# Kernel optimization log

Measured on AMD Instinct MI355X. Metric: run time of the kernel, lower is better.

Reference implementation:

```python
import jax, jax.numpy as jnp
import numpy as np
from jax import lax

KH, KW = 3, 3  # hardcoded in the original extract_patches sizes=(1,3,3,1)


def setup_inputs() -> dict:
    key = jax.random.key(0)
    k1, k2, k3 = jax.random.split(key, 3)
    B, H, W, C = 32, 56, 56, 128
    num_och = 256
    x = jax.random.normal(k1, (B, H, W, C), dtype=jnp.float32)
    w = jax.random.normal(k2, (num_och, KH * KW * C), dtype=jnp.float32) * 0.05
    b = jax.random.normal(k3, (num_och,), dtype=jnp.float32) * 0.05
    return {"x": x, "w": w, "b": b}


def reference(x, w, b):
    # Original: extract_patches (SAME, stride 1, 3x3) -> tile num_och times ->
    # elementwise multiply with w -> reduce_sum over patch axis -> + bias.
    # This is exactly a 3x3 SAME conv: patch layout is (ky, kx, cin) row-major,
    # matching tf.image.extract_patches depth ordering.
    num_och = w.shape[0]
    cin = x.shape[-1]
    # (num_och, KH*KW*C) -> (KH, KW, C, num_och) for HWIO kernel layout
    kernel = w.reshape(num_och, KH, KW, cin).transpose(1, 2, 3, 0)
    out = lax.conv_general_dilated(
        x, kernel,
        window_strides=(1, 1),
        padding="SAME",
        dimension_numbers=("NHWC", "HWIO", "NHWC"),
    )
    return out + b
```

## Files before the change

kernel.cpp:

```cpp
#include <hip/hip_runtime.h>
#include <hip/hip_bf16.h>

#define HH   56
#define WW_  56
#define CIN  128
#define OCH  256
#define NPIX (32*56*56)
#define NX   (NPIX*CIN)
#define NW   (OCH*9*CIN)
#define XB_BYTES ((size_t)NX*2)
#define WB_BYTES ((size_t)NW*2)
#define ZP_OFF   (XB_BYTES + WB_BYTES)
#define WS_NEEDED (ZP_OFF + 256)

#define NT   18
#define SLOT 32768
#define THREADS 512

typedef __attribute__((ext_vector_type(8))) short bf16x8;
typedef __attribute__((ext_vector_type(4))) float f32x4;
typedef __attribute__((address_space(1))) void v_g;
typedef __attribute__((address_space(3))) void v_l;

__device__ __forceinline__ unsigned short f2bf(float f) {
  union { float f; unsigned u; } v; v.f = f;
  unsigned r = v.u + 0x7FFF + ((v.u >> 16) & 1);
  return (unsigned short)(r >> 16);
}

__global__ __launch_bounds__(256) void convert_kern(
    const float* __restrict__ x, const float* __restrict__ w,
    char* __restrict__ ws)
{
  if (blockIdx.x == 0 && threadIdx.x < 64)
    ((float*)(ws + ZP_OFF))[threadIdx.x] = 0.f;

  unsigned short* out = (unsigned short*)ws;
  const int NT8 = (NX + NW) / 8;
  for (int i = blockIdx.x * blockDim.x + threadIdx.x; i < NT8;
       i += gridDim.x * blockDim.x) {
    const int e = i * 8;
    const float* src = (e < NX) ? (x + e) : (w + (e - NX));
    const float4 a = ((const float4*)src)[0];
    const float4 b = ((const float4*)src)[1];
    union { bf16x8 v; unsigned short u[8]; } p;
    p.u[0] = f2bf(a.x); p.u[1] = f2bf(a.y); p.u[2] = f2bf(a.z); p.u[3] = f2bf(a.w);
    p.u[4] = f2bf(b.x); p.u[5] = f2bf(b.y); p.u[6] = f2bf(b.z); p.u[7] = f2bf(b.w);
    *(bf16x8*)(out + e) = p.v;
  }
}

__global__ __launch_bounds__(THREADS, 2) void conv_gemm3(
    const char* __restrict__ ws, const float* __restrict__ bias,
    float* __restrict__ out)
{
  __shared__ char lds[3 * SLOT];

  const char* xb = ws;
  const char* wb = ws + XB_BYTES;
  const char* zp = ws + ZP_OFF;

  const int tid  = threadIdx.x;
  const int lane = tid & 63;
  const int m0   = (blockIdx.x >> 1) * 128;
  const int n0   = (blockIdx.x & 1) * 128;

  const int r0  = tid >> 3;
  const int chk = ((tid & 7) ^ (r0 & 7)) * 16;
  const char* zpc = zp + chk;

  int pixA[2], phA[2], pwA[2];
  const char* bsrc[2];
#pragma unroll
  for (int l = 0; l < 2; ++l) {
    const int r  = r0 + l * 64;
    const int p  = m0 + r;
    const int pb = p / 3136;
    const int phw = p - pb * 3136;
    phA[l] = phw / 56;
    pwA[l] = phw - phA[l] * 56;
    pixA[l] = p;
    bsrc[l] = wb + (size_t)(n0 + r) * 2304 + chk;
  }

  const int fr = lane & 15;
  const int fq = lane >> 4;
  const int wv = tid >> 6;
  const int wr = wv >> 2;
  const int wc = wv & 3;

  int aoff[2][4], boff[2][2];
#pragma unroll
  for (int ks = 0; ks < 2; ++ks) {
#pragma unroll
    for (int mi = 0; mi < 4; ++mi) {
      const int r = wr * 64 + mi * 16 + fr;
      aoff[ks][mi] = r * 128 + ((ks * 64 + fq * 16) ^ ((r & 7) << 4));
    }
#pragma unroll
    for (int nj = 0; nj < 2; ++nj) {
      const int c = wc * 32 + nj * 16 + fr;
      boff[ks][nj] = 16384 + c * 128 + ((ks * 64 + fq * 16) ^ ((c & 7) << 4));
    }
  }

  f32x4 acc[4][2];
  const f32x4 zero4 = {0.f, 0.f, 0.f, 0.f};
#pragma unroll
  for (int mi = 0; mi < 4; ++mi)
#pragma unroll
    for (int nj = 0; nj < 2; ++nj) acc[mi][nj] = zero4;

#define STAGE(tt, dst) do {                                                   \
    const int kpos_ = (tt) >> 1, kh_ = (tt) & 1;                              \
    const int ky_ = kpos_ / 3;                                                \
    const int dy_ = ky_ - 1, dx_ = kpos_ - ky_ * 3 - 1;                       \
    _Pragma("unroll")                                                         \
    for (int l = 0; l < 2; ++l) {                                             \
      const int ih_ = phA[l] + dy_, iw_ = pwA[l] + dx_;                       \
      const bool v_ = ((unsigned)ih_ < 56u) & ((unsigned)iw_ < 56u);          \
      const char* ga_ = v_ ? (xb + (size_t)(pixA[l] + dy_ * 56 + dx_) * 256   \
                                 + kh_ * 128 + chk)                           \
                           : zpc;                                             \
      __builtin_amdgcn_global_load_lds((const v_g*)ga_,                       \
          (v_l*)((dst) + l * 8192 + tid * 16), 16, 0, 0);                     \
    }                                                                         \
    _Pragma("unroll")                                                         \
    for (int l = 0; l < 2; ++l)                                               \
      __builtin_amdgcn_global_load_lds((const v_g*)(bsrc[l] + (tt) * 128),    \
          (v_l*)((dst) + 16384 + l * 8192 + tid * 16), 16, 0, 0);             \
  } while (0)

#define COMPUTE(src) do {                                                     \
    bf16x8 Af[2][4], Bf[2][2];                                                \
    _Pragma("unroll")                                                         \
    for (int ks = 0; ks < 2; ++ks) {                                          \
      _Pragma("unroll")                                                       \
      for (int mi = 0; mi < 4; ++mi)                                          \
        Af[ks][mi] = *(const bf16x8*)((src) + aoff[ks][mi]);                  \
      _Pragma("unroll")                                                       \
      for (int nj = 0; nj < 2; ++nj)                                          \
        Bf[ks][nj] = *(const bf16x8*)((src) + boff[ks][nj]);                  \
    }                                                                         \
    __builtin_amdgcn_s_setprio(1);                                            \
    _Pragma("unroll")                                                         \
    for (int ks = 0; ks < 2; ++ks)                                            \
      _Pragma("unroll")                                                       \
      for (int mi = 0; mi < 4; ++mi)                                          \
        _Pragma("unroll")                                                     \
        for (int nj = 0; nj < 2; ++nj)                                        \
          acc[mi][nj] = __builtin_amdgcn_mfma_f32_16x16x32_bf16(              \
              Af[ks][mi], Bf[ks][nj], acc[mi][nj], 0, 0, 0);                  \
    __builtin_amdgcn_s_setprio(0);                                            \
  } while (0)

  char* p0 = lds;
  char* p1 = lds + SLOT;
  char* p2 = lds + 2 * SLOT;

  STAGE(0, p0);
  STAGE(1, p1);

#pragma unroll
  for (int t = 0; t < NT - 2; ++t) {
    __builtin_amdgcn_s_barrier();
    __builtin_amdgcn_sched_barrier(0);
    STAGE(t + 2, p2);
    asm volatile("s_waitcnt vmcnt(8)" ::: "memory");
    __builtin_amdgcn_s_barrier();
    __builtin_amdgcn_sched_barrier(0);
    COMPUTE(p0);
    char* tmp = p0; p0 = p1; p1 = p2; p2 = tmp;
  }

  asm volatile("s_waitcnt vmcnt(4)" ::: "memory");
  __builtin_amdgcn_s_barrier();
  __builtin_amdgcn_sched_barrier(0);
  COMPUTE(p0);
  { char* tmp = p0; p0 = p1; p1 = p2; p2 = tmp; }

  asm volatile("s_waitcnt vmcnt(0)" ::: "memory");
  __builtin_amdgcn_s_barrier();
  __builtin_amdgcn_sched_barrier(0);
  COMPUTE(p0);

#undef STAGE
#undef COMPUTE

  float bv[2];
#pragma unroll
  for (int nj = 0; nj < 2; ++nj) bv[nj] = bias[n0 + wc * 32 + nj * 16 + fr];

#pragma unroll
  for (int mi = 0; mi < 4; ++mi) {
#pragma unroll
    for (int j = 0; j < 4; ++j) {
      const int prow = m0 + wr * 64 + mi * 16 + fq * 4 + j;
      float* orow = out + (size_t)prow * OCH + n0 + wc * 32 + fr;
#pragma unroll
      for (int nj = 0; nj < 2; ++nj)
        orow[nj * 16] = acc[mi][nj][j] + bv[nj];
    }
  }
}

__global__ __launch_bounds__(256) void conv3x3_mfma_fb(
    const float* __restrict__ x, const float* __restrict__ w,
    const float* __restrict__ bias, float* __restrict__ out)
{
  __shared__ alignas(16) unsigned char As[128 * 64];
  __shared__ alignas(16) unsigned char Bs[128 * 64];

  const int tid = threadIdx.x;
  const int m0 = (blockIdx.x >> 1) * 128;
  const int n0 = (blockIdx.x & 1) * 128;

  const int srow = tid >> 1;
  const int soff = (tid & 1) * 16;

  const int p   = m0 + srow;
  const int pb  = p / (HH * WW_);
  const int phw = p - pb * (HH * WW_);
  const int ph  = phw / WW_;
  const int pw  = phw - ph * WW_;

  const float* xrow = x + ((size_t)((pb * HH + ph) * WW_ + pw)) * CIN + soff;
  const float* wrow = w + (size_t)(n0 + srow) * (9 * CIN) + soff;

  const int sw0 = (srow * 64 + soff * 2)      ^ ((srow & 7) << 4);
  const int sw1 = (srow * 64 + soff * 2 + 16) ^ ((srow & 7) << 4);

  const int lane = tid & 63;
  const int wv = tid >> 6;
  const int wm = (wv >> 1) * 64;
  const int wn = (wv & 1) * 64;
  const int fr = lane & 15;
  const int fq = lane >> 4;

  int aoff[4], boff[4];
#pragma unroll
  for (int i = 0; i < 4; ++i) {
    const int r = wm + i * 16 + fr;
    aoff[i] = (r * 64 + fq * 16) ^ ((r & 7) << 4);
    const int c = wn + i * 16 + fr;
    boff[i] = (c * 64 + fq * 16) ^ ((c & 7) << 4);
  }

  f32x4 acc[4][4];
  const f32x4 zero4 = {0.f, 0.f, 0.f, 0.f};
#pragma unroll
  for (int i = 0; i < 4; ++i)
#pragma unroll
    for (int j = 0; j < 4; ++j) acc[i][j] = zero4;

#pragma unroll 1
  for (int kpos = 0; kpos < 9; ++kpos) {
    const int ky = kpos / 3;
    const int kx = kpos - ky * 3;
    const int ih = ph + ky - 1;
    const int iw = pw + kx - 1;
    const bool valid = ((unsigned)ih < (unsigned)HH) & ((unsigned)iw < (unsigned)WW_);
    const float* asrc = xrow + ((ky - 1) * WW_ + (kx - 1)) * CIN;
    const float* bsrc2 = wrow + kpos * CIN;

#pragma unroll 1
    for (int kc = 0; kc < 4; ++kc) {
      float4 a0, a1, a2, a3;
      if (valid) {
        const float4* s = (const float4*)(asrc + kc * 32);
        a0 = s[0]; a1 = s[1]; a2 = s[2]; a3 = s[3];
      } else {
        a0 = make_float4(0.f, 0.f, 0.f, 0.f);
        a1 = a0; a2 = a0; a3 = a0;
      }
      const float4* tql = (const float4*)(bsrc2 + kc * 32);
      const float4 b0 = tql[0], b1 = tql[1], b2 = tql[2], b3 = tql[3];

      __syncthreads();

      union { bf16x8 v; unsigned short u[8]; } pA0, pA1, pB0, pB1;
      pA0.u[0] = f2bf(a0.x); pA0.u[1] = f2bf(a0.y); pA0.u[2] = f2bf(a0.z); pA0.u[3] = f2bf(a0.w);
      pA0.u[4] = f2bf(a1.x); pA0.u[5] = f2bf(a1.y); pA0.u[6] = f2bf(a1.z); pA0.u[7] = f2bf(a1.w);
      pA1.u[0] = f2bf(a2.x); pA1.u[1] = f2bf(a2.y); pA1.u[2] = f2bf(a2.z); pA1.u[3] = f2bf(a2.w);
      pA1.u[4] = f2bf(a3.x); pA1.u[5] = f2bf(a3.y); pA1.u[6] = f2bf(a3.z); pA1.u[7] = f2bf(a3.w);
      pB0.u[0] = f2bf(b0.x); pB0.u[1] = f2bf(b0.y); pB0.u[2] = f2bf(b0.z); pB0.u[3] = f2bf(b0.w);
      pB0.u[4] = f2bf(b1.x); pB0.u[5] = f2bf(b1.y); pB0.u[6] = f2bf(b1.z); pB0.u[7] = f2bf(b1.w);
      pB1.u[0] = f2bf(b2.x); pB1.u[1] = f2bf(b2.y); pB1.u[2] = f2bf(b2.z); pB1.u[3] = f2bf(b2.w);
      pB1.u[4] = f2bf(b3.x); pB1.u[5] = f2bf(b3.y); pB1.u[6] = f2bf(b3.z); pB1.u[7] = f2bf(b3.w);

      *(bf16x8*)(As + sw0) = pA0.v;
      *(bf16x8*)(As + sw1) = pA1.v;
      *(bf16x8*)(Bs + sw0) = pB0.v;
      *(bf16x8*)(Bs + sw1) = pB1.v;

      __syncthreads();

      bf16x8 af[4], bfr[4];
#pragma unroll
      for (int i = 0; i < 4; ++i) af[i]  = *(const bf16x8*)(As + aoff[i]);
#pragma unroll
      for (int j = 0; j < 4; ++j) bfr[j] = *(const bf16x8*)(Bs + boff[j]);
#pragma unroll
      for (int i = 0; i < 4; ++i)
#pragma unroll
        for (int j = 0; j < 4; ++j)
          acc[i][j] = __builtin_amdgcn_mfma_f32_16x16x32_bf16(af[i], bfr[j], acc[i][j], 0, 0, 0);
    }
  }

  float bv[4];
#pragma unroll
  for (int j = 0; j < 4; ++j) bv[j] = bias[n0 + wn + j * 16 + fr];

#pragma unroll
  for (int mi = 0; mi < 4; ++mi) {
#pragma unroll
    for (int j = 0; j < 4; ++j) {
      const int prow = m0 + wm + mi * 16 + fq * 4 + j;
      float* orow = out + (size_t)prow * OCH + n0 + wn + fr;
#pragma unroll
      for (int ni = 0; ni < 4; ++ni)
        orow[ni * 16] = acc[mi][ni][j] + bv[ni];
    }
  }
}

extern "C" void kernel_launch(void* const* d_in, const int* in_sizes, int n_in,
                              void* d_out, int out_size, void* d_ws, size_t ws_size,
                              hipStream_t stream) {
  (void)in_sizes; (void)n_in; (void)out_size;
  const float* x = (const float*)d_in[0];
  const float* w = (const float*)d_in[1];
  const float* b = (const float*)d_in[2];
  float* out = (float*)d_out;

  const int grid = (NPIX / 128) * 2;
  if (ws_size >= WS_NEEDED) {
    convert_kern<<<dim3(2048), dim3(256), 0, stream>>>(x, w, (char*)d_ws);
    conv_gemm3<<<dim3(grid), dim3(THREADS), 0, stream>>>((const char*)d_ws, b, out);
  } else {
    conv3x3_mfma_fb<<<dim3(grid), dim3(256), 0, stream>>>(x, w, b, out);
  }
}
```

Measured before the change: 211.6 us.

## Use 256x256 output tiles with 1024-thread blocks and double buffering

Each block now covers 256 pixels by all 256 output channels with 16 waves, using 1024 threads instead of 512 and a 4x4 MFMA accumulator tile per wave. This halves the number of times the activation patches are loaded and raises MFMA work per LDS read. The LDS pipeline drops from three stages to two with larger 64KB slots, and block indices are remapped across 8 groups to improve L2 locality. The cost is fewer blocks per CU, a shallower prefetch pipeline and higher register pressure.

```diff
diff --git a/kernel.cpp b/kernel.cpp
--- a/kernel.cpp
+++ b/kernel.cpp
@@ -14,8 +14,8 @@
 #define WS_NEEDED (ZP_OFF + 256)
 
 #define NT   18
-#define SLOT 32768
-#define THREADS 512
+#define SLOT 65536
+#define THREADS 1024
 
 typedef __attribute__((ext_vector_type(8))) short bf16x8;
 typedef __attribute__((ext_vector_type(4))) float f32x4;
@@ -50,11 +50,11 @@
   }
 }
 
-__global__ __launch_bounds__(THREADS, 2) void conv_gemm3(
+__global__ __launch_bounds__(THREADS) void conv_gemm4(
     const char* __restrict__ ws, const float* __restrict__ bias,
     float* __restrict__ out)
 {
-  __shared__ char lds[3 * SLOT];
+  __shared__ char lds[2 * SLOT];
 
   const char* xb = ws;
   const char* wb = ws + XB_BYTES;
@@ -62,8 +62,9 @@
 
   const int tid  = threadIdx.x;
   const int lane = tid & 63;
-  const int m0   = (blockIdx.x >> 1) * 128;
-  const int n0   = (blockIdx.x & 1) * 128;
+
+  const int bid = blockIdx.x;
+  const int m0  = ((bid & 7) * 49 + (bid >> 3)) * 256;
 
   const int r0  = tid >> 3;
   const int chk = ((tid & 7) ^ (r0 & 7)) * 16;
@@ -73,14 +74,13 @@
   const char* bsrc[2];
 #pragma unroll
   for (int l = 0; l < 2; ++l) {
-    const int r  = r0 + l * 64;
-    const int p  = m0 + r;
+    const int p  = m0 + r0 + l * 128;
     const int pb = p / 3136;
     const int phw = p - pb * 3136;
     phA[l] = phw / 56;
     pwA[l] = phw - phA[l] * 56;
     pixA[l] = p;
-    bsrc[l] = wb + (size_t)(n0 + r) * 2304 + chk;
+    bsrc[l] = wb + (size_t)(r0 + l * 128) * 2304 + chk;
   }
 
   const int fr = lane & 15;
@@ -89,7 +89,7 @@
   const int wr = wv >> 2;
   const int wc = wv & 3;
 
-  int aoff[2][4], boff[2][2];
+  int aoff[2][4], boff[2][4];
 #pragma unroll
   for (int ks = 0; ks < 2; ++ks) {
 #pragma unroll
@@ -98,18 +98,18 @@
       aoff[ks][mi] = r * 128 + ((ks * 64 + fq * 16) ^ ((r & 7) << 4));
     }
 #pragma unroll
-    for (int nj = 0; nj < 2; ++nj) {
-      const int c = wc * 32 + nj * 16 + fr;
-      boff[ks][nj] = 16384 + c * 128 + ((ks * 64 + fq * 16) ^ ((c & 7) << 4));
-    }
-  }
-
-  f32x4 acc[4][2];
+    for (int nj = 0; nj < 4; ++nj) {
+      const int c = wc * 64 + nj * 16 + fr;
+      boff[ks][nj] = 32768 + c * 128 + ((ks * 64 + fq * 16) ^ ((c & 7) << 4));
+    }
+  }
+
+  f32x4 acc[4][4];
   const f32x4 zero4 = {0.f, 0.f, 0.f, 0.f};
 #pragma unroll
   for (int mi = 0; mi < 4; ++mi)
 #pragma unroll
-    for (int nj = 0; nj < 2; ++nj) acc[mi][nj] = zero4;
+    for (int nj = 0; nj < 4; ++nj) acc[mi][nj] = zero4;
 
 #define STAGE(tt, dst) do {                                                   \
     const int kpos_ = (tt) >> 1, kh_ = (tt) & 1;                              \
@@ -123,82 +123,71 @@
                                  + kh_ * 128 + chk)                           \
                            : zpc;                                             \
       __builtin_amdgcn_global_load_lds((const v_g*)ga_,                       \
-          (v_l*)((dst) + l * 8192 + tid * 16), 16, 0, 0);                     \
+          (v_l*)((dst) + l * 16384 + tid * 16), 16, 0, 0);                    \
     }                                                                         \
     _Pragma("unroll")                                                         \
     for (int l = 0; l < 2; ++l)                                               \
       __builtin_amdgcn_global_load_lds((const v_g*)(bsrc[l] + (tt) * 128),    \
-          (v_l*)((dst) + 16384 + l * 8192 + tid * 16), 16, 0, 0);             \
+          (v_l*)((dst) + 32768 + l * 16384 + tid * 16), 16, 0, 0);            \
   } while (0)
 
 #define COMPUTE(src) do {                                                     \
-    bf16x8 Af[2][4], Bf[2][2];                                                \
     _Pragma("unroll")                                                         \
     for (int ks = 0; ks < 2; ++ks) {                                          \
+      bf16x8 Af[4], Bf[4];                                                    \
       _Pragma("unroll")                                                       \
       for (int mi = 0; mi < 4; ++mi)                                          \
-        Af[ks][mi] = *(const bf16x8*)((src) + aoff[ks][mi]);                  \
+        Af[mi] = *(const bf16x8*)((src) + aoff[ks][mi]);                      \
       _Pragma("unroll")                                                       \
-      for (int nj = 0; nj < 2; ++nj)                                          \
-        Bf[ks][nj] = *(const bf16x8*)((src) + boff[ks][nj]);                  \
-    }                                                                         \
-    __builtin_amdgcn_s_setprio(1);                                            \
-    _Pragma("unroll")                                                         \
-    for (int ks = 0; ks < 2; ++ks)                                            \
+      for (int nj = 0; nj < 4; ++nj)                                          \
+        Bf[nj] = *(const bf16x8*)((src) + boff[ks][nj]);                      \
+      __builtin_amdgcn_s_setprio(1);                                          \
       _Pragma("unroll")                                                       \
       for (int mi = 0; mi < 4; ++mi)                                          \
         _Pragma("unroll")                                                     \
-        for (int nj = 0; nj < 2; ++nj)                                        \
+        for (int nj = 0; nj < 4; ++nj)                                        \
           acc[mi][nj] = __builtin_amdgcn_mfma_f32_16x16x32_bf16(              \
-              Af[ks][mi], Bf[ks][nj], acc[mi][nj], 0, 0, 0);                  \
-    __builtin_amdgcn_s_setprio(0);                                            \
+              Af[mi], Bf[nj], acc[mi][nj], 0, 0, 0);                          \
+      __builtin_amdgcn_s_setprio(0);                                          \
+    }                                                                         \
   } while (0)
 
-  char* p0 = lds;
-  char* p1 = lds + SLOT;
-  char* p2 = lds + 2 * SLOT;
-
-  STAGE(0, p0);
-  STAGE(1, p1);
-
-#pragma unroll
-  for (int t = 0; t < NT - 2; ++t) {
+  char* s0 = lds;
+  char* s1 = lds + SLOT;
+
+  STAGE(0, s0);
+
+#pragma unroll
+  for (int t = 0; t < NT - 1; ++t) {
     __builtin_amdgcn_s_barrier();
     __builtin_amdgcn_sched_barrier(0);
-    STAGE(t + 2, p2);
-    asm volatile("s_waitcnt vmcnt(8)" ::: "memory");
+    STAGE(t + 1, ((t + 1) & 1) ? s1 : s0);
+    asm volatile("s_waitcnt vmcnt(4)" ::: "memory");
     __builtin_amdgcn_s_barrier();
     __builtin_amdgcn_sched_barrier(0);
-    COMPUTE(p0);
-    char* tmp = p0; p0 = p1; p1 = p2; p2 = tmp;
-  }
-
-  asm volatile("s_waitcnt vmcnt(4)" ::: "memory");
-  __builtin_amdgcn_s_barrier();
-  __builtin_amdgcn_sched_barrier(0);
-  COMPUTE(p0);
-  { char* tmp = p0; p0 = p1; p1 = p2; p2 = tmp; }
+    COMPUTE((t & 1) ? s1 : s0);
+  }
 
   asm volatile("s_waitcnt vmcnt(0)" ::: "memory");
   __builtin_amdgcn_s_barrier();
   __builtin_amdgcn_sched_barrier(0);
-  COMPUTE(p0);
+  COMPUTE(((NT - 1) & 1) ? s1 : s0);
 
 #undef STAGE
 #undef COMPUTE
 
-  float bv[2];
-#pragma unroll
-  for (int nj = 0; nj < 2; ++nj) bv[nj] = bias[n0 + wc * 32 + nj * 16 + fr];
+  float bv[4];
+#pragma unroll
+  for (int nj = 0; nj < 4; ++nj) bv[nj] = bias[wc * 64 + nj * 16 + fr];
 
 #pragma unroll
   for (int mi = 0; mi < 4; ++mi) {
 #pragma unroll
     for (int j = 0; j < 4; ++j) {
       const int prow = m0 + wr * 64 + mi * 16 + fq * 4 + j;
-      float* orow = out + (size_t)prow * OCH + n0 + wc * 32 + fr;
-#pragma unroll
-      for (int nj = 0; nj < 2; ++nj)
+      float* orow = out + (size_t)prow * OCH + wc * 64 + fr;
+#pragma unroll
+      for (int nj = 0; nj < 4; ++nj)
         orow[nj * 16] = acc[mi][nj][j] + bv[nj];
     }
   }
@@ -334,11 +323,11 @@
   const float* b = (const float*)d_in[2];
   float* out = (float*)d_out;
 
-  const int grid = (NPIX / 128) * 2;
   if (ws_size >= WS_NEEDED) {
     convert_kern<<<dim3(2048), dim3(256), 0, stream>>>(x, w, (char*)d_ws);
-    conv_gemm3<<<dim3(grid), dim3(THREADS), 0, stream>>>((const char*)d_ws, b, out);
+    const int grid = NPIX / 256;
+    conv_gemm4<<<dim3(grid), dim3(THREADS), 0, stream>>>((const char*)d_ws, b, out);
   } else {
-    conv3x3_mfma_fb<<<dim3(grid), dim3(256), 0, stream>>>(x, w, b, out);
-  }
-}
+    conv3x3_mfma_fb<<<dim3((NPIX / 128) * 2), dim3(256), 0, stream>>>(x, w, b, out);
+  }
+}
```

New measurement: 215.1 us. Within noise of the previous version (+1.7%).
